# Optimization experiments

Measured on AMD Instinct MI355X. Metric: run time of the kernel, lower is better.

Reference implementation:

```python
import jax, jax.numpy as jnp
import numpy as np

B, C, H, W = 2, 64, 256, 256
G = 4  # groups in ResB convs


def _bn(x, g, b, m, v, eps=1e-5):
    inv = g / jnp.sqrt(v + eps)
    return x * inv[None, :, None, None] + (b - m * inv)[None, :, None, None]


def _gconv(x, w, b):
    y = jax.lax.conv_general_dilated(x, w, (1, 1), ((1, 1), (1, 1)),
                                     feature_group_count=G,
                                     dimension_numbers=('NCHW', 'OIHW', 'NCHW'))
    return y + b[None, :, None, None]


def _resb(x, w1, b1, w2, b2):
    h = jax.nn.leaky_relu(_gconv(x, w1, b1), 0.1)
    return _gconv(h, w2, b2) + x


def _conv1x1(x, w, b):
    return jnp.einsum('bchw,oc->bohw', x, w[:, :, 0, 0]) + b[None, :, None, None]


def _m_relax(M, num_pixels=2):
    # sum of M shifted by +/-1..num_pixels along the row (query) axis, zero padded
    out = M
    for i in range(1, num_pixels + 1):
        out = out + jnp.pad(M[:, :-i, :], ((0, 0), (i, 0), (0, 0)))
        out = out + jnp.pad(M[:, i:, :], ((0, 0), (0, i), (0, 0)))
    return out


def setup_inputs() -> dict:
    key = jax.random.key(0)
    ks = jax.random.split(key, 8)
    f = lambda k, shape, s=1.0: jax.random.normal(k, shape, dtype=jnp.float32) * s
    return {
        'x_left': f(ks[0], (B, C, H, W)),
        'x_right': f(ks[1], (B, C, H, W)),
        'catfea_left': f(ks[2], (B, C, H, W)),
        'catfea_right': f(ks[3], (B, C, H, W)),
        'bn_gamma': jnp.ones((C,), jnp.float32),
        'bn_beta': jnp.zeros((C,), jnp.float32),
        'bn_mean': jnp.zeros((C,), jnp.float32),
        'bn_var': jnp.ones((C,), jnp.float32),
        'rb_w1': f(ks[4], (C, C // G, 3, 3), 0.05),
        'rb_b1': jnp.zeros((C,), jnp.float32),
        'rb_w2': f(ks[5], (C, C // G, 3, 3), 0.05),
        'rb_b2': jnp.zeros((C,), jnp.float32),
        'bq_w': f(ks[6], (C, C, 1, 1), 0.05),
        'bq_b': jnp.zeros((C,), jnp.float32),
        'bs_w': f(ks[7], (C, C, 1, 1), 0.05),
        'bs_b': jnp.zeros((C,), jnp.float32),
    }


def reference(x_left, x_right, catfea_left, catfea_right,
              bn_gamma, bn_beta, bn_mean, bn_var,
              rb_w1, rb_b1, rb_w2, rb_b2,
              bq_w, bq_b, bs_w, bs_b):
    b, c0, h, w = x_left.shape

    Q = _conv1x1(_resb(_bn(x_left, bn_gamma, bn_beta, bn_mean, bn_var),
                       rb_w1, rb_b1, rb_w2, rb_b2), bq_w, bq_b)
    Q = Q - jnp.mean(Q, axis=3, keepdims=True)
    K = _conv1x1(_resb(_bn(x_right, bn_gamma, bn_beta, bn_mean, bn_var),
                       rb_w1, rb_b1, rb_w2, rb_b2), bs_w, bs_b)
    K = K - jnp.mean(K, axis=3, keepdims=True)

    c = Q.shape[1]
    # [b*h, w, c] and [b*h, c, w]  (w == w_size)
    Qr = Q.transpose(0, 2, 3, 1).reshape(-1, w, c)
    Kr = K.transpose(0, 2, 1, 3).reshape(-1, c, w)
    score = jnp.einsum('nic,ncj->nij', Qr, Kr)

    M_r2l = jax.nn.softmax(score, axis=-1)
    M_l2r = jax.nn.softmax(score.transpose(0, 2, 1), axis=-1)

    M_r2l_relaxed = _m_relax(M_r2l, 2)
    V_left = jax.lax.stop_gradient(
        jnp.einsum('nij,nji->ni', M_r2l_relaxed, M_l2r)).reshape(b, 1, h, w)
    M_l2r_relaxed = _m_relax(M_l2r, 2)
    V_right = jax.lax.stop_gradient(
        jnp.einsum('nij,nji->ni', M_l2r_relaxed, M_r2l)).reshape(b, 1, h, w)

    V_left_t = jnp.tanh(5.0 * V_left)
    V_right_t = jnp.tanh(5.0 * V_right)

    xr = x_right.transpose(0, 2, 3, 1).reshape(-1, w, c0)
    xl = x_left.transpose(0, 2, 3, 1).reshape(-1, w, c0)
    x_leftT = jnp.einsum('nij,njc->nic', M_r2l, xr).reshape(b, h, w, c0).transpose(0, 3, 1, 2)
    x_rightT = jnp.einsum('nij,njc->nic', M_l2r, xl).reshape(b, h, w, c0).transpose(0, 3, 1, 2)

    out_left = x_left * (1.0 - V_left_t) + x_leftT * V_left_t
    out_right = x_right * (1.0 - V_right_t) + x_rightT * V_right_t
    return out_left, out_right
```

## Files before the change

kernel.cpp:

```cpp
#include <hip/hip_runtime.h>
#include <math.h>

#define CC 64
#define HH 256
#define WW 256
#define GC 16
#define HWp (HH*WW)
#define LOG2E 1.44269504088896340736f

typedef __attribute__((ext_vector_type(8))) short short8;
typedef __attribute__((ext_vector_type(4))) float f32x4;
typedef __attribute__((ext_vector_type(2))) unsigned long u64x2;

static constexpr size_t OFS_BNSS = 0;
static constexpr size_t OFS_W1H  = 512;
static constexpr size_t OFS_W1L  = 20992;
static constexpr size_t OFS_W2H  = 41472;
static constexpr size_t OFS_W2L  = 61952;
static constexpr size_t OFS_WQH  = 82432;
static constexpr size_t OFS_WQL  = 98816;
static constexpr size_t OFS_WSH  = 115200;
static constexpr size_t OFS_WSL  = 131584;
static constexpr size_t OFS_RMAX = 147968;
static constexpr size_t OFS_RINV = OFS_RMAX + 524288;
static constexpr size_t OFS_CMAX = OFS_RINV + 524288;
static constexpr size_t OFS_CINV = OFS_CMAX + 524288;
static constexpr size_t OFS_XBNH = OFS_CINV + 524288;
static constexpr size_t HALO_BYTES = (size_t)2*258*258*64*2;
static constexpr size_t OFS_XBNL = OFS_XBNH + HALO_BYTES;
static constexpr size_t OFS_HH   = OFS_XBNL + HALO_BYTES;
static constexpr size_t OFS_HL   = OFS_HH   + HALO_BYTES;
static constexpr size_t OFS_QH   = OFS_HL   + HALO_BYTES;
static constexpr size_t QK_BYTES = (size_t)512*256*64*2;
static constexpr size_t OFS_QL   = OFS_QH + QK_BYTES;
static constexpr size_t OFS_KH   = OFS_QL + QK_BYTES;
static constexpr size_t OFS_KL   = OFS_KH + QK_BYTES;

__device__ __forceinline__ unsigned short f2bf(float v) {
    unsigned int u = __float_as_uint(v);
    return (unsigned short)((u + 0x7fffu + ((u >> 16) & 1u)) >> 16);
}
__device__ __forceinline__ float bf2f(unsigned short h) {
    return __uint_as_float(((unsigned int)h) << 16);
}

__global__ __launch_bounds__(256) void wprep(const float* __restrict__ g, const float* __restrict__ be,
        const float* __restrict__ mn, const float* __restrict__ va,
        const float* __restrict__ w1, const float* __restrict__ w2,
        const float* __restrict__ wq, const float* __restrict__ wsW,
        float* __restrict__ bnss,
        unsigned short* __restrict__ w1h, unsigned short* __restrict__ w1l,
// ... 16 lines not shown
        }
        unsigned short h1 = f2bf(v1), h2 = f2bf(v2);
        w1h[idx] = h1; w1l[idx] = f2bf(v1 - bf2f(h1));
        w2h[idx] = h2; w2l[idx] = f2bf(v2 - bf2f(h2));
    }
    for (int idx = t; idx < 64*128; idx += 256) {
        int oc = idx >> 7, k = idx & 127;
        float vq = wq[oc*64 + (k & 63)];
        float vs = wsW[oc*64 + (k & 63)];
        unsigned short hq = f2bf(vq), hs = f2bf(vs);
        wqh[idx] = hq; wql[idx] = f2bf(vq - bf2f(hq));
        wsh[idx] = hs; wsl[idx] = f2bf(vs - bf2f(hs));
    }
}

__global__ void zero_k(u64x2* __restrict__ p, size_t n) {
    size_t i = (size_t)blockIdx.x*blockDim.x + threadIdx.x;
    size_t st = (size_t)gridDim.x*blockDim.x;
    for (; i < n; i += st) p[i] = (u64x2){0ul, 0ul};
}

__global__ __launch_bounds__(256) void prep_k(const float* __restrict__ x,
        const float* __restrict__ bnss,
        unsigned short* __restrict__ xh, unsigned short* __restrict__ xl) {
    __shared__ float ld[64*256];
    __shared__ float sc[64], sh[64];
    int blk = blockIdx.x;
    int y = blk & 255, b = blk >> 8;
    int t = threadIdx.x;
    if (t < 64) { sc[t] = bnss[t]; sh[t] = bnss[64+t]; }
    for (int idx = t; idx < 16384; idx += 256) {
        int c = idx >> 8, xx = idx & 255;
        ld[c*256 + xx] = x[((size_t)(b*64 + c)*256 + y)*256 + xx];
    }
    __syncthreads();
    int px = t;
    size_t base = ((size_t)(b*258 + y+1)*258 + px+1)*64;
    #pragma unroll
    for (int ch = 0; ch < 4; ++ch) {
        short8 h0, h1, l0, l1;
        #pragma unroll
        for (int j = 0; j < 8; ++j) {
            int c = ch*16 + j;
            float f = ld[c*256 + px]*sc[c] + sh[c];
            unsigned short hh = f2bf(f);
            h0[j] = (short)hh; l0[j] = (short)f2bf(f - bf2f(hh));
        }
        #pragma unroll
        for (int j = 0; j < 8; ++j) {
            int c = ch*16 + 8 + j;
            float f = ld[c*256 + px]*sc[c] + sh[c];
            unsigned short hh = f2bf(f);
            h1[j] = (short)hh; l1[j] = (short)f2bf(f - bf2f(hh));
        }
        *(short8*)(xh + base + ch*16)     = h0;
        *(short8*)(xh + base + ch*16 + 8) = h1;
        *(short8*)(xl + base + ch*16)     = l0;
        *(short8*)(xl + base + ch*16 + 8) = l1;
    }
}

__global__ __launch_bounds__(256) void conv1_m(
        const unsigned short* __restrict__ inh, const unsigned short* __restrict__ inl,
        const unsigned short* __restrict__ wth, const unsigned short* __restrict__ wtl,
        const float* __restrict__ bias,
        unsigned short* __restrict__ oh, unsigned short* __restrict__ ol) {
    __shared__ unsigned short lh[256*72];
    __shared__ unsigned short ll[256*72];
    int blk = blockIdx.x;
    int y = blk & 255, b = blk >> 8;
    int t = threadIdx.x;
    int w = t >> 6, l = t & 63;
    int lr = l & 15, lg = l >> 4;

    f32x4 acc[4][4];
    #pragma unroll
    for (int g = 0; g < 4; ++g) {
        float bb = bias[g*16 + lr];
        #pragma unroll
        for (int mt = 0; mt < 4; ++mt) acc[mt][g] = (f32x4){bb,bb,bb,bb};
    }
    size_t lanebase = ((size_t)(b*258 + y)*258 + 64*w + lr)*64 + (lg & 1)*8;
    int koff[5];
    #pragma unroll
    for (int ks = 0; ks < 5; ++ks) {
        int tap = 2*ks + (lg >> 1);
        if (tap > 8) tap = 8;
        koff[ks] = ((tap/3)*258 + (tap%3))*64;
    }
    #pragma unroll
    for (int ks = 0; ks < 5; ++ks) {
        #pragma unroll
        for (int g = 0; g < 4; ++g) {
            short8 bh = *(const short8*)(wth + (g*16+lr)*160 + ks*32 + lg*8);
            short8 bl = *(const short8*)(wtl + (g*16+lr)*160 + ks*32 + lg*8);
            #pragma unroll
            for (int mt = 0; mt < 4; ++mt) {
                size_t off = lanebase + koff[ks] + mt*1024 + g*16;
                short8 ah = *(const short8*)(inh + off);
                short8 al = *(const short8*)(inl + off);
                acc[mt][g] = __builtin_amdgcn_mfma_f32_16x16x32_bf16(ah, bh, acc[mt][g], 0,0,0);
                acc[mt][g] = __builtin_amdgcn_mfma_f32_16x16x32_bf16(ah, bl, acc[mt][g], 0,0,0);
                acc[mt][g] = __builtin_amdgcn_mfma_f32_16x16x32_bf16(al, bh, acc[mt][g], 0,0,0);
            }
        }
    }
    #pragma unroll
    for (int mt = 0; mt < 4; ++mt)
        #pragma unroll
        for (int g = 0; g < 4; ++g)
            #pragma unroll
            for (int r = 0; r < 4; ++r) {
                float v = acc[mt][g][r];
                v = v > 0.f ? v : 0.1f*v;
                int px = 64*w + mt*16 + lg*4 + r;
                int oc = g*16 + lr;
                unsigned short hh = f2bf(v);
                lh[px*72 + oc] = hh;
                ll[px*72 + oc] = f2bf(v - bf2f(hh));
            }
    __syncthreads();
    size_t rowbase = ((size_t)(b*258 + y+1)*258 + 1)*64;
    #pragma unroll
    for (int i = 0; i < 8; ++i) {
        int cid = i*256 + t;
        int px = cid >> 3, part = cid & 7;
        *(short8*)(oh + rowbase + (size_t)px*64 + part*8) = *(short8*)&lh[px*72 + part*8];
        *(short8*)(ol + rowbase + (size_t)px*64 + part*8) = *(short8*)&ll[px*72 + part*8];
    }
}

__global__ __launch_bounds__(256) void conv2_m(
        const unsigned short* __restrict__ hh, const unsigned short* __restrict__ hl,
        const unsigned short* __restrict__ xbh, const unsigned short* __restrict__ xbl,
        const unsigned short* __restrict__ wth, const unsigned short* __restrict__ wtl,
        const float* __restrict__ bias2,
        const unsigned short* __restrict__ wph, const unsigned short* __restrict__ wpl,
        const float* __restrict__ biasq, float scaleOut,
        unsigned short* __restrict__ Qh, unsigned short* __restrict__ Ql) {
    __shared__ unsigned short rs[4*9216];
    __shared__ float red2[256];
    __shared__ float meanl[64];
    int blk = blockIdx.x;
    int y = blk & 255, b = blk >> 8;
    int t = threadIdx.x;
    int w = t >> 6, l = t & 63;
    int lr = l & 15, lg = l >> 4;

    f32x4 acc[4][4];
    #pragma unroll
    for (int g = 0; g < 4; ++g) {
        float bb = bias2[g*16 + lr];
        #pragma unroll
        for (int mt = 0; mt < 4; ++mt) acc[mt][g] = (f32x4){bb,bb,bb,bb};
    }
    size_t lanebase = ((size_t)(b*258 + y)*258 + 64*w + lr)*64 + (lg & 1)*8;
    int koff[5];
    #pragma unroll
    for (int ks = 0; ks < 5; ++ks) {
        int tap = 2*ks + (lg >> 1);
        if (tap > 8) tap = 8;
        koff[ks] = ((tap/3)*258 + (tap%3))*64;
    }
    #pragma unroll
    for (int ks = 0; ks < 5; ++ks) {
        #pragma unroll
        for (int g = 0; g < 4; ++g) {
            short8 bh = *(const short8*)(wth + (g*16+lr)*160 + ks*32 + lg*8);
            short8 bl = *(const short8*)(wtl + (g*16+lr)*160 + ks*32 + lg*8);
            #pragma unroll
            for (int mt = 0; mt < 4; ++mt) {
                size_t off = lanebase + koff[ks] + mt*1024 + g*16;
                short8 ah = *(const short8*)(hh + off);
                short8 al = *(const short8*)(hl + off);
                acc[mt][g] = __builtin_amdgcn_mfma_f32_16x16x32_bf16(ah, bh, acc[mt][g], 0,0,0);
                acc[mt][g] = __builtin_amdgcn_mfma_f32_16x16x32_bf16(ah, bl, acc[mt][g], 0,0,0);
                acc[mt][g] = __builtin_amdgcn_mfma_f32_16x16x32_bf16(al, bh, acc[mt][g], 0,0,0);
            }
        }
    }
    unsigned short* rsw = rs + w*9216;
    #pragma unroll
    for (int mt = 0; mt < 4; ++mt)
        #pragma unroll
        for (int g = 0; g < 4; ++g)
            #pragma unroll
            for (int r = 0; r < 4; ++r) {
                float v = acc[mt][g][r];
                int pxl = mt*16 + lg*4 + r;
                int oc = g*16 + lr;
                unsigned short hv = f2bf(v);
                rsw[pxl*72 + oc] = hv;
                rsw[4608 + pxl*72 + oc] = f2bf(v - bf2f(hv));
            }
    f32x4 acc2[4][4];
    #pragma unroll
    for (int nt = 0; nt < 4; ++nt) {
        float bb = biasq[nt*16 + lr];
        #pragma unroll
        for (int mt = 0; mt < 4; ++mt) acc2[mt][nt] = (f32x4){bb,bb,bb,bb};
    }
    size_t cbase = ((size_t)(b*258 + y+1)*258 + 64*w + lr + 1)*64 + lg*8;
    #pragma unroll
    for (int ks = 0; ks < 4; ++ks) {
        short8 Ah[4], Al[4];
        #pragma unroll
        for (int mt = 0; mt < 4; ++mt) {
            if (ks < 2) {
                Ah[mt] = *(short8*)&rsw[(mt*16+lr)*72 + ks*32 + lg*8];
                Al[mt] = *(short8*)&rsw[4608 + (mt*16+lr)*72 + ks*32 + lg*8];
            } else {
                size_t off = cbase + (size_t)mt*1024 + (ks-2)*32;
                Ah[mt] = *(const short8*)(xbh + off);
                Al[mt] = *(const short8*)(xbl + off);
            }
        }
        #pragma unroll
        for (int nt = 0; nt < 4; ++nt) {
            short8 Bh = *(const short8*)(wph + (nt*16+lr)*128 + ks*32 + lg*8);
            short8 Bl = *(const short8*)(wpl + (nt*16+lr)*128 + ks*32 + lg*8);
            #pragma unroll
            for (int mt = 0; mt < 4; ++mt) {
                acc2[mt][nt] = __builtin_amdgcn_mfma_f32_16x16x32_bf16(Ah[mt], Bh, acc2[mt][nt], 0,0,0);
                acc2[mt][nt] = __builtin_amdgcn_mfma_f32_16x16x32_bf16(Ah[mt], Bl, acc2[mt][nt], 0,0,0);
                acc2[mt][nt] = __builtin_amdgcn_mfma_f32_16x16x32_bf16(Al[mt], Bh, acc2[mt][nt], 0,0,0);
            }
        }
    }
    __syncthreads();
    float* qs = (float*)rs;
    #pragma unroll
    for (int mt = 0; mt < 4; ++mt)
        #pragma unroll
        for (int nt = 0; nt < 4; ++nt)
            #pragma unroll
            for (int r = 0; r < 4; ++r)
                qs[(64*w + mt*16 + lg*4 + r)*68 + nt*16 + lr] = acc2[mt][nt][r];
    __syncthreads();
    {
        int c = t & 63, seg = t >> 6;
        float s = 0.f;
        for (int i = 0; i < 64; ++i) s += qs[(seg*64 + i)*68 + c];
        red2[t] = s;
    }
    __syncthreads();
    if (t < 64) meanl[t] = (red2[t] + red2[64+t] + red2[128+t] + red2[192+t]) * (1.f/256.f);
    __syncthreads();
    int n = b*256 + y;
    size_t obase = ((size_t)n*256 + t)*64;
    #pragma unroll
    for (int ch = 0; ch < 4; ++ch) {
        short8 h0, h1, l0, l1;
        #pragma unroll
        for (int j = 0; j < 8; ++j) {
            int c = ch*16 + j;
            float f = (qs[t*68 + c] - meanl[c]) * scaleOut;
            unsigned short hv = f2bf(f);
            h0[j] = (short)hv; l0[j] = (short)f2bf(f - bf2f(hv));
        }
        #pragma unroll
        for (int j = 0; j < 8; ++j) {
            int c = ch*16 + 8 + j;
            float f = (qs[t*68 + c] - meanl[c]) * scaleOut;
            unsigned short hv = f2bf(f);
            h1[j] = (short)hv; l1[j] = (short)f2bf(f - bf2f(hv));
        }
        *(short8*)(Qh + obase + ch*16)     = h0;
        *(short8*)(Qh + obase + ch*16 + 8) = h1;
        *(short8*)(Ql + obase + ch*16)     = l0;
        *(short8*)(Ql + obase + ch*16 + 8) = l1;
    }
}

__global__ __launch_bounds__(256) void s1_stats(
        const unsigned short* __restrict__ Qhi, const unsigned short* __restrict__ Qlo,
        const unsigned short* __restrict__ Khi, const unsigned short* __restrict__ Klo,
        float* __restrict__ rmax, float* __restrict__ rinv,
        float* __restrict__ cmax, float* __restrict__ cinv) {
    __shared__ float colred[4][256][2];
    int n = blockIdx.x;
    int t = threadIdx.x;
    int w = t >> 6, l = t & 63;
    int lr = l & 15, lg = l >> 4;
    const size_t qb = (size_t)n * 16384;

    short8 qh[4][2], ql[4][2];
    #pragma unroll
    for (int rf = 0; rf < 4; ++rf)
        #pragma unroll
        for (int ks = 0; ks < 2; ++ks) {
            size_t a = qb + (size_t)(w*64 + rf*16 + lr)*64 + ks*32 + lg*8;
            qh[rf][ks] = *reinterpret_cast<const short8*>(Qhi + a);
            ql[rf][ks] = *reinterpret_cast<const short8*>(Qlo + a);
        }
    float mrow[4][4], srow[4][4];
    #pragma unroll
    for (int rf = 0; rf < 4; ++rf)
        #pragma unroll
        for (int r = 0; r < 4; ++r) { mrow[rf][r] = -3.0e38f; srow[rf][r] = 0.f; }

    for (int jt = 0; jt < 8; ++jt) {
        short8 kh[2][2], kl[2][2];
        #pragma unroll
        for (int cf = 0; cf < 2; ++cf)
            #pragma unroll
            for (int ks = 0; ks < 2; ++ks) {
                size_t a = qb + (size_t)(jt*32 + cf*16 + lr)*64 + ks*32 + lg*8;
                kh[cf][ks] = *reinterpret_cast<const short8*>(Khi + a);
                kl[cf][ks] = *reinterpret_cast<const short8*>(Klo + a);
            }
        f32x4 acc[4][2];
        #pragma unroll
        for (int rf = 0; rf < 4; ++rf)
            #pragma unroll
            for (int cf = 0; cf < 2; ++cf) acc[rf][cf] = (f32x4){0.f,0.f,0.f,0.f};
        #pragma unroll
        for (int ks = 0; ks < 2; ++ks)
            #pragma unroll
            for (int rf = 0; rf < 4; ++rf)
                #pragma unroll
                for (int cf = 0; cf < 2; ++cf) {
                    acc[rf][cf] = __builtin_amdgcn_mfma_f32_16x16x32_bf16(qh[rf][ks], kh[cf][ks], acc[rf][cf], 0,0,0);
                    acc[rf][cf] = __builtin_amdgcn_mfma_f32_16x16x32_bf16(qh[rf][ks], kl[cf][ks], acc[rf][cf], 0,0,0);
                    acc[rf][cf] = __builtin_amdgcn_mfma_f32_16x16x32_bf16(ql[rf][ks], kh[cf][ks], acc[rf][cf], 0,0,0);
                }
        #pragma unroll
        for (int rf = 0; rf < 4; ++rf)
            #pragma unroll
            for (int r = 0; r < 4; ++r) {
                float e0 = acc[rf][0][r], e1 = acc[rf][1][r];
                float m2 = fmaxf(mrow[rf][r], fmaxf(e0, e1));
                srow[rf][r] = srow[rf][r]*exp2f(mrow[rf][r]-m2) + exp2f(e0-m2) + exp2f(e1-m2);
                mrow[rf][r] = m2;
            }
        #pragma unroll
        for (int cf = 0; cf < 2; ++cf) {
            float m = acc[0][cf][0];
            #pragma unroll
            for (int rf = 0; rf < 4; ++rf)
                #pragma unroll
                for (int r = 0; r < 4; ++r) m = fmaxf(m, acc[rf][cf][r]);
            float s = 0.f;
            #pragma unroll
            for (int rf = 0; rf < 4; ++rf)
                #pragma unroll
                for (int r = 0; r < 4; ++r) s += exp2f(acc[rf][cf][r] - m);
            #pragma unroll
            for (int mask = 16; mask <= 32; mask <<= 1) {
                float om = __shfl_xor(m, mask);
                float os = __shfl_xor(s, mask);
                float m2 = fmaxf(m, om);
                s = s*exp2f(m-m2) + os*exp2f(om-m2);
                m = m2;
            }
            if (lg == 0) {
                int j = jt*32 + cf*16 + lr;
                colred[w][j][0] = m;
                colred[w][j][1] = s;
            }
        }
    }
    #pragma unroll
    for (int rf = 0; rf < 4; ++rf)
        #pragma unroll
        for (int r = 0; r < 4; ++r) {
            float m = mrow[rf][r], s = srow[rf][r];
            #pragma unroll
            for (int mask = 1; mask <= 8; mask <<= 1) {
                float om = __shfl_xor(m, mask);
                float os = __shfl_xor(s, mask);
                float m2 = fmaxf(m, om);
                s = s*exp2f(m-m2) + os*exp2f(om-m2);
                m = m2;
            }
            if (lr == 0) {
                int row = w*64 + rf*16 + lg*4 + r;
                rmax[n*256 + row] = m;
                rinv[n*256 + row] = 1.f / s;
            }
        }
    __syncthreads();
    {
        int j = t;
        float m = colred[0][j][0], s = colred[0][j][1];
        #pragma unroll
        for (int w2_ = 1; w2_ < 4; ++w2_) {
            float om = colred[w2_][j][0], os = colred[w2_][j][1];
            float m2 = fmaxf(m, om);
            s = s*exp2f(m-m2) + os*exp2f(om-m2);
            m = m2;
        }
        cmax[n*256 + j] = m;
        cinv[n*256 + j] = 1.f / s;
    }
}

__global__ __launch_bounds__(256) void s23_apply(
        const unsigned short* __restrict__ Ahi, const unsigned short* __restrict__ Alo,
        const unsigned short* __restrict__ Bhi, const unsigned short* __restrict__ Blo,
        const float* __restrict__ rowmax, const float* __restrict__ rowinv,
        const float* __restrict__ colmax, const float* __restrict__ colinv,
        const float* __restrict__ Xpv, const float* __restrict__ Xblend,
        float* __restrict__ outp) {
    __shared__ unsigned short pa[256][40];
    __shared__ unsigned short pb[256][40];
    __shared__ float vred[4][256];
    __shared__ float cmax_l[256], cinv_l[256];
    __shared__ float vfin[256];
    int n = blockIdx.x;
    int y = n & 255, b = n >> 8;
    int t = threadIdx.x;
    int w = t >> 6, l = t & 63;
    int lr = l & 15, lg = l >> 4;
    const size_t qb = (size_t)n * 16384;

    cmax_l[t] = colmax[n*256 + t];
    cinv_l[t] = colinv[n*256 + t];
    for (int q = t; q < 1024; q += 256) ((float*)vred)[q] = 0.f;

    float rmx[4][4], rin[4][4];
    #pragma unroll
    for (int rf = 0; rf < 4; ++rf)
        #pragma unroll
        for (int r = 0; r < 4; ++r) {
            int row = w*64 + rf*16 + lg*4 + r;
            rmx[rf][r] = rowmax[n*256 + row];
            rin[rf][r] = rowinv[n*256 + row];
        }
    short8 ah[4][2], al[4][2];
    #pragma unroll
    for (int rf = 0; rf < 4; ++rf)
        #pragma unroll
        for (int ks = 0; ks < 2; ++ks) {
            size_t a = qb + (size_t)(w*64 + rf*16 + lr)*64 + ks*32 + lg*8;
            ah[rf][ks] = *reinterpret_cast<const short8*>(Ahi + a);
            al[rf][ks] = *reinterpret_cast<const short8*>(Alo + a);
        }
    f32x4 pv[4][4];
    #pragma unroll
    for (int rf = 0; rf < 4; ++rf)
        #pragma unroll
        for (int cf = 0; cf < 4; ++cf) pv[rf][cf] = (f32x4){0.f,0.f,0.f,0.f};
    float vacc[6];
    #pragma unroll
    for (int s = 0; s < 6; ++s) vacc[s] = 0.f;

    const float* xpvb = Xpv + (size_t)b*CC*HWp + (size_t)y*WW;
    __syncthreads();

    for (int jt = 0; jt < 8; ++jt) {
        short8 bh[2][2], bl[2][2];
        #pragma unroll
        for (int cf = 0; cf < 2; ++cf)
            #pragma unroll
            for (int ks = 0; ks < 2; ++ks) {
                size_t a = qb + (size_t)(jt*32 + cf*16 + lr)*64 + ks*32 + lg*8;
                bh[cf][ks] = *reinterpret_cast<const short8*>(Bhi + a);
                bl[cf][ks] = *reinterpret_cast<const short8*>(Blo + a);
            }
        f32x4 acc[4][2];
        #pragma unroll
        for (int rf = 0; rf < 4; ++rf)
            #pragma unroll
            for (int cf = 0; cf < 2; ++cf) acc[rf][cf] = (f32x4){0.f,0.f,0.f,0.f};
        #pragma unroll
        for (int ks = 0; ks < 2; ++ks)
            #pragma unroll
            for (int rf = 0; rf < 4; ++rf)
                #pragma unroll
                for (int cf = 0; cf < 2; ++cf) {
                    acc[rf][cf] = __builtin_amdgcn_mfma_f32_16x16x32_bf16(ah[rf][ks], bh[cf][ks], acc[rf][cf], 0,0,0);
                    acc[rf][cf] = __builtin_amdgcn_mfma_f32_16x16x32_bf16(ah[rf][ks], bl[cf][ks], acc[rf][cf], 0,0,0);
                    acc[rf][cf] = __builtin_amdgcn_mfma_f32_16x16x32_bf16(al[rf][ks], bh[cf][ks], acc[rf][cf], 0,0,0);
                }
        #pragma unroll
        for (int rf = 0; rf < 4; ++rf)
            #pragma unroll
            for (int cf = 0; cf < 2; ++cf) {
                int col = cf*16 + lr;
                float cm = cmax_l[jt*32 + col];
                float ci = cinv_l[jt*32 + col];
                #pragma unroll
                for (int r = 0; r < 4; ++r) {
                    float e = acc[rf][cf][r];
                    int row = w*64 + rf*16 + lg*4 + r;
                    pa[row][col] = f2bf(exp2f(e - rmx[rf][r]) * rin[rf][r]);
                    pb[row][col] = f2bf(exp2f(e - cm) * ci);
                }
            }
        __syncthreads();
        #pragma unroll
        for (int Tl = 0; Tl < 4; ++Tl) {
            int T = w*4 + Tl;
            short8 afr = *reinterpret_cast<short8*>(&pa[T*16 + lr][lg*8]);
            #pragma unroll
            for (int dT = -1; dT <= 1; ++dT) {
                int Tp = T + dT;
                if (Tp < 0 || Tp > 15) continue;
                short8 bfr = *reinterpret_cast<short8*>(&pb[Tp*16 + lr][lg*8]);
                f32x4 wacc = (f32x4){0.f,0.f,0.f,0.f};
                wacc = __builtin_amdgcn_mfma_f32_16x16x32_bf16(afr, bfr, wacc, 0,0,0);
                #pragma unroll
                for (int r = 0; r < 4; ++r) {
                    int diff = lg*4 + r - lr - 16*dT;
                    if (diff >= -2 && diff <= 2) vacc[Tl + dT + 1] += wacc[r];
                }
            }
        }
        #pragma unroll
        for (int cf4 = 0; cf4 < 4; ++cf4) {
            const float* xp = xpvb + (size_t)(cf4*16 + lr)*HWp + jt*32 + lg*8;
            float4 xv0 = *(const float4*)(xp);
            float4 xv1 = *(const float4*)(xp + 4);
            short8 xf;
            xf[0] = (short)f2bf(xv0.x); xf[1] = (short)f2bf(xv0.y);
            xf[2] = (short)f2bf(xv0.z); xf[3] = (short)f2bf(xv0.w);
            xf[4] = (short)f2bf(xv1.x); xf[5] = (short)f2bf(xv1.y);
            xf[6] = (short)f2bf(xv1.z); xf[7] = (short)f2bf(xv1.w);
            #pragma unroll
            for (int rf = 0; rf < 4; ++rf) {
                short8 paf = *reinterpret_cast<short8*>(&pa[w*64 + rf*16 + lr][lg*8]);
                pv[rf][cf4] = __builtin_amdgcn_mfma_f32_16x16x32_bf16(paf, xf, pv[rf][cf4], 0,0,0);
            }
        }
        __syncthreads();
    }
    #pragma unroll
    for (int s = 0; s < 6; ++s) {
        float v = vacc[s];
        v += __shfl_xor(v, 16);
        v += __shfl_xor(v, 32);
        if (lg == 0) {
            int i = (w*4 - 1 + s)*16 + lr;
            if (i >= 0 && i < 256) vred[w][i] = v;
        }
    }
    __syncthreads();
    vfin[t] = tanhf(5.f * (vred[0][t] + vred[1][t] + vred[2][t] + vred[3][t]));
    __syncthreads();
    const float* xbb = Xblend + (size_t)b*CC*HWp + (size_t)y*WW;
    float* ob = outp + (size_t)b*CC*HWp + (size_t)y*WW;
    #pragma unroll
    for (int rf = 0; rf < 4; ++rf)
        #pragma unroll
        for (int r = 0; r < 4; ++r) {
            int row = w*64 + rf*16 + lg*4 + r;
            float vt = vfin[row];
            #pragma unroll
            for (int cf4 = 0; cf4 < 4; ++cf4) {
                int c = cf4*16 + lr;
                size_t ga = (size_t)c*HWp + row;
                float xv = xbb[ga];
                ob[ga] = xv + vt * (pv[rf][cf4][r] - xv);
            }
        }
}

extern "C" void kernel_launch(void* const* d_in, const int* in_sizes, int n_in,
                              void* d_out, int out_size, void* d_ws, size_t ws_size,
                              hipStream_t stream) {
    const float* x_left  = (const float*)d_in[0];
    const float* x_right = (const float*)d_in[1];
    const float* bn_g = (const float*)d_in[4];
    const float* bn_b = (const float*)d_in[5];
    const float* bn_m = (const float*)d_in[6];
    const float* bn_v = (const float*)d_in[7];
    const float* w1  = (const float*)d_in[8];
    const float* b1  = (const float*)d_in[9];
// ... 14 lines not shown
    unsigned short* wql = (unsigned short*)(base + OFS_WQL);
    unsigned short* wsh = (unsigned short*)(base + OFS_WSH);
    unsigned short* wsl = (unsigned short*)(base + OFS_WSL);
    float* rmaxp = (float*)(base + OFS_RMAX);
    float* rinvp = (float*)(base + OFS_RINV);
    float* cmaxp = (float*)(base + OFS_CMAX);
    float* cinvp = (float*)(base + OFS_CINV);
    unsigned short* xbh = (unsigned short*)(base + OFS_XBNH);
    unsigned short* xbl = (unsigned short*)(base + OFS_XBNL);
    unsigned short* hh  = (unsigned short*)(base + OFS_HH);
    unsigned short* hl  = (unsigned short*)(base + OFS_HL);
    unsigned short* Qh  = (unsigned short*)(base + OFS_QH);
    unsigned short* Ql  = (unsigned short*)(base + OFS_QL);
    unsigned short* Kh  = (unsigned short*)(base + OFS_KH);
    unsigned short* Kl  = (unsigned short*)(base + OFS_KL);

    float* outl = (float*)d_out;
    float* outr = outl + (size_t)2*CC*HWp;

    hipLaunchKernelGGL(wprep, dim3(1), dim3(256), 0, stream,
                       bn_g, bn_b, bn_m, bn_v, w1, w2, bqw, bsw,
                       bnss, w1h, w1l, w2h, w2l, wqh, wql, wsh, wsl);
    hipLaunchKernelGGL(zero_k, dim3(2048), dim3(256), 0, stream,
                       (u64x2*)(base + OFS_XBNH), (size_t)(4*HALO_BYTES/16));
    hipLaunchKernelGGL(prep_k,  dim3(512), dim3(256), 0, stream, x_left, bnss, xbh, xbl);
    hipLaunchKernelGGL(conv1_m, dim3(512), dim3(256), 0, stream, xbh, xbl, w1h, w1l, b1, hh, hl);
    hipLaunchKernelGGL(conv2_m, dim3(512), dim3(256), 0, stream, hh, hl, xbh, xbl,
                       w2h, w2l, b2, wqh, wql, bqb, LOG2E, Qh, Ql);
    hipLaunchKernelGGL(prep_k,  dim3(512), dim3(256), 0, stream, x_right, bnss, xbh, xbl);
    hipLaunchKernelGGL(conv1_m, dim3(512), dim3(256), 0, stream, xbh, xbl, w1h, w1l, b1, hh, hl);
    hipLaunchKernelGGL(conv2_m, dim3(512), dim3(256), 0, stream, hh, hl, xbh, xbl,
                       w2h, w2l, b2, wsh, wsl, bsb, 1.0f, Kh, Kl);
    hipLaunchKernelGGL(s1_stats, dim3(512), dim3(256), 0, stream, Qh, Ql, Kh, Kl, rmaxp, rinvp, cmaxp, cinvp);
    hipLaunchKernelGGL(s23_apply, dim3(512), dim3(256), 0, stream,
                       Qh, Ql, Kh, Kl, rmaxp, rinvp, cmaxp, cinvp, x_right, x_left, outl);
    hipLaunchKernelGGL(s23_apply, dim3(512), dim3(256), 0, stream,
                       Kh, Kl, Qh, Ql, cmaxp, cinvp, rmaxp, rinvp, x_left, x_right, outr);
}
```

Before: 703.6 us.

## Use 512-thread blocks, zero only halo borders, precompute bf16 inputs for PV

```diff
diff --git a/kernel.cpp b/kernel.cpp
--- a/kernel.cpp
+++ b/kernel.cpp
@@ -10,7 +10,6 @@
 
 typedef __attribute__((ext_vector_type(8))) short short8;
 typedef __attribute__((ext_vector_type(4))) float f32x4;
-typedef __attribute__((ext_vector_type(2))) unsigned long u64x2;
 
 static constexpr size_t OFS_BNSS = 0;
 static constexpr size_t OFS_W1H  = 512;
@@ -27,6 +26,7 @@
 static constexpr size_t OFS_CINV = OFS_CMAX + 524288;
 static constexpr size_t OFS_XBNH = OFS_CINV + 524288;
 static constexpr size_t HALO_BYTES = (size_t)2*258*258*64*2;
+static constexpr size_t HALO_U16  = HALO_BYTES/2;
 static constexpr size_t OFS_XBNL = OFS_XBNH + HALO_BYTES;
 static constexpr size_t OFS_HH   = OFS_XBNL + HALO_BYTES;
 static constexpr size_t OFS_HL   = OFS_HH   + HALO_BYTES;
@@ -35,6 +35,9 @@
 static constexpr size_t OFS_QL   = OFS_QH + QK_BYTES;
 static constexpr size_t OFS_KH   = OFS_QL + QK_BYTES;
 static constexpr size_t OFS_KL   = OFS_KH + QK_BYTES;
+static constexpr size_t XB_BYTES = (size_t)2*64*256*256*2;
+static constexpr size_t OFS_XLB  = OFS_KL + QK_BYTES;
+static constexpr size_t OFS_XRB  = OFS_XLB + XB_BYTES;
 
 __device__ __forceinline__ unsigned short f2bf(float v) {
     unsigned int u = __float_as_uint(v);
@@ -81,53 +84,68 @@
     }
 }
 
-__global__ void zero_k(u64x2* __restrict__ p, size_t n) {
-    size_t i = (size_t)blockIdx.x*blockDim.x + threadIdx.x;
-    size_t st = (size_t)gridDim.x*blockDim.x;
-    for (; i < n; i += st) p[i] = (u64x2){0ul, 0ul};
-}
-
-__global__ __launch_bounds__(256) void prep_k(const float* __restrict__ x,
+__global__ __launch_bounds__(256) void zhalo(unsigned short* __restrict__ p) {
+    int idx = blockIdx.x*256 + threadIdx.x;
+    if (idx >= 65792) return;
+    int ch8 = idx & 7;
+    int rest = idx >> 3;
+    int slab = rest / 1028;
+    int pos  = rest % 1028;
+    size_t slabbase = (size_t)slab * 4260096;
+    int y, x;
+    if (pos < 258)      { y = 0;   x = pos; }
+    else if (pos < 516) { y = 257; x = pos - 258; }
+    else if (pos < 772) { y = pos - 516 + 1; x = 0; }
+    else                { y = pos - 772 + 1; x = 257; }
+    size_t off = slabbase + ((size_t)y*258 + x)*64 + ch8*8;
+    *(short8*)(p + off) = (short8){0,0,0,0,0,0,0,0};
+}
+
+__global__ __launch_bounds__(512) void prep_k(const float* __restrict__ x,
         const float* __restrict__ bnss,
-        unsigned short* __restrict__ xh, unsigned short* __restrict__ xl) {
+        unsigned short* __restrict__ xh, unsigned short* __restrict__ xl,
+        unsigned short* __restrict__ xb16) {
     __shared__ float ld[64*256];
     __shared__ float sc[64], sh[64];
     int blk = blockIdx.x;
     int y = blk & 255, b = blk >> 8;
     int t = threadIdx.x;
     if (t < 64) { sc[t] = bnss[t]; sh[t] = bnss[64+t]; }
-    for (int idx = t; idx < 16384; idx += 256) {
+    for (int idx = t; idx < 16384; idx += 512) {
         int c = idx >> 8, xx = idx & 255;
-        ld[c*256 + xx] = x[((size_t)(b*64 + c)*256 + y)*256 + xx];
-    }
-    __syncthreads();
-    int px = t;
+        float v = x[((size_t)(b*64 + c)*256 + y)*256 + xx];
+        ld[c*256 + xx] = v;
+        xb16[((size_t)(b*64 + c)*256 + y)*256 + xx] = f2bf(v);
+    }
+    __syncthreads();
+    int px = t >> 1, half = (t & 1) * 32;
     size_t base = ((size_t)(b*258 + y+1)*258 + px+1)*64;
     #pragma unroll
-    for (int ch = 0; ch < 4; ++ch) {
+    for (int cc = 0; cc < 2; ++cc) {
+        int cb = half + cc*16;
         short8 h0, h1, l0, l1;
         #pragma unroll
         for (int j = 0; j < 8; ++j) {
-            int c = ch*16 + j;
+            int c = cb + j;
             float f = ld[c*256 + px]*sc[c] + sh[c];
             unsigned short hh = f2bf(f);
             h0[j] = (short)hh; l0[j] = (short)f2bf(f - bf2f(hh));
         }
         #pragma unroll
         for (int j = 0; j < 8; ++j) {
-            int c = ch*16 + 8 + j;
+            int c = cb + 8 + j;
             float f = ld[c*256 + px]*sc[c] + sh[c];
             unsigned short hh = f2bf(f);
             h1[j] = (short)hh; l1[j] = (short)f2bf(f - bf2f(hh));
         }
-        *(short8*)(xh + base + ch*16)     = h0;
-        *(short8*)(xh + base + ch*16 + 8) = h1;
-        *(short8*)(xl + base + ch*16)     = l0;
-        *(short8*)(xl + base + ch*16 + 8) = l1;
-    }
-}
-
-__global__ __launch_bounds__(256) void conv1_m(
+        *(short8*)(xh + base + cb)     = h0;
+        *(short8*)(xh + base + cb + 8) = h1;
+        *(short8*)(xl + base + cb)     = l0;
+        *(short8*)(xl + base + cb + 8) = l1;
+    }
+}
+
+__global__ __launch_bounds__(512) void conv1_m(
         const unsigned short* __restrict__ inh, const unsigned short* __restrict__ inl,
         const unsigned short* __restrict__ wth, const unsigned short* __restrict__ wtl,
         const float* __restrict__ bias,
@@ -140,14 +158,14 @@
     int w = t >> 6, l = t & 63;
     int lr = l & 15, lg = l >> 4;
 
-    f32x4 acc[4][4];
+    f32x4 acc[2][4];
     #pragma unroll
     for (int g = 0; g < 4; ++g) {
         float bb = bias[g*16 + lr];
         #pragma unroll
-        for (int mt = 0; mt < 4; ++mt) acc[mt][g] = (f32x4){bb,bb,bb,bb};
-    }
-    size_t lanebase = ((size_t)(b*258 + y)*258 + 64*w + lr)*64 + (lg & 1)*8;
+        for (int mt = 0; mt < 2; ++mt) acc[mt][g] = (f32x4){bb,bb,bb,bb};
+    }
+    size_t lanebase = ((size_t)(b*258 + y)*258 + 32*w + lr)*64 + (lg & 1)*8;
     int koff[5];
     #pragma unroll
     for (int ks = 0; ks < 5; ++ks) {
@@ -162,7 +180,7 @@
             short8 bh = *(const short8*)(wth + (g*16+lr)*160 + ks*32 + lg*8);
             short8 bl = *(const short8*)(wtl + (g*16+lr)*160 + ks*32 + lg*8);
             #pragma unroll
-            for (int mt = 0; mt < 4; ++mt) {
+            for (int mt = 0; mt < 2; ++mt) {
                 size_t off = lanebase + koff[ks] + mt*1024 + g*16;
                 short8 ah = *(const short8*)(inh + off);
                 short8 al = *(const short8*)(inl + off);
@@ -173,14 +191,14 @@
         }
     }
     #pragma unroll
-    for (int mt = 0; mt < 4; ++mt)
+    for (int mt = 0; mt < 2; ++mt)
         #pragma unroll
         for (int g = 0; g < 4; ++g)
             #pragma unroll
             for (int r = 0; r < 4; ++r) {
                 float v = acc[mt][g][r];
                 v = v > 0.f ? v : 0.1f*v;
-                int px = 64*w + mt*16 + lg*4 + r;
+                int px = 32*w + mt*16 + lg*4 + r;
                 int oc = g*16 + lr;
                 unsigned short hh = f2bf(v);
                 lh[px*72 + oc] = hh;
@@ -189,15 +207,15 @@
     __syncthreads();
     size_t rowbase = ((size_t)(b*258 + y+1)*258 + 1)*64;
     #pragma unroll
-    for (int i = 0; i < 8; ++i) {
-        int cid = i*256 + t;
+    for (int i = 0; i < 4; ++i) {
+        int cid = i*512 + t;
         int px = cid >> 3, part = cid & 7;
         *(short8*)(oh + rowbase + (size_t)px*64 + part*8) = *(short8*)&lh[px*72 + part*8];
         *(short8*)(ol + rowbase + (size_t)px*64 + part*8) = *(short8*)&ll[px*72 + part*8];
     }
 }
 
-__global__ __launch_bounds__(256) void conv2_m(
+__global__ __launch_bounds__(512) void conv2_m(
         const unsigned short* __restrict__ hh, const unsigned short* __restrict__ hl,
         const unsigned short* __restrict__ xbh, const unsigned short* __restrict__ xbl,
         const unsigned short* __restrict__ wth, const unsigned short* __restrict__ wtl,
@@ -205,8 +223,8 @@
         const unsigned short* __restrict__ wph, const unsigned short* __restrict__ wpl,
         const float* __restrict__ biasq, float scaleOut,
         unsigned short* __restrict__ Qh, unsigned short* __restrict__ Ql) {
-    __shared__ unsigned short rs[4*9216];
-    __shared__ float red2[256];
+    __shared__ unsigned short rs[8*4608];
+    __shared__ float red2[512];
     __shared__ float meanl[64];
     int blk = blockIdx.x;
     int y = blk & 255, b = blk >> 8;
@@ -214,14 +232,14 @@
     int w = t >> 6, l = t & 63;
     int lr = l & 15, lg = l >> 4;
 
-    f32x4 acc[4][4];
+    f32x4 acc[2][4];
     #pragma unroll
     for (int g = 0; g < 4; ++g) {
         float bb = bias2[g*16 + lr];
         #pragma unroll
-        for (int mt = 0; mt < 4; ++mt) acc[mt][g] = (f32x4){bb,bb,bb,bb};
-    }
-    size_t lanebase = ((size_t)(b*258 + y)*258 + 64*w + lr)*64 + (lg & 1)*8;
+        for (int mt = 0; mt < 2; ++mt) acc[mt][g] = (f32x4){bb,bb,bb,bb};
+    }
+    size_t lanebase = ((size_t)(b*258 + y)*258 + 32*w + lr)*64 + (lg & 1)*8;
     int koff[5];
     #pragma unroll
     for (int ks = 0; ks < 5; ++ks) {
@@ -236,7 +254,7 @@
             short8 bh = *(const short8*)(wth + (g*16+lr)*160 + ks*32 + lg*8);
             short8 bl = *(const short8*)(wtl + (g*16+lr)*160 + ks*32 + lg*8);
             #pragma unroll
-            for (int mt = 0; mt < 4; ++mt) {
+            for (int mt = 0; mt < 2; ++mt) {
                 size_t off = lanebase + koff[ks] + mt*1024 + g*16;
                 short8 ah = *(const short8*)(hh + off);
                 short8 al = *(const short8*)(hl + off);
@@ -246,9 +264,9 @@
             }
         }
     }
-    unsigned short* rsw = rs + w*9216;
-    #pragma unroll
-    for (int mt = 0; mt < 4; ++mt)
+    unsigned short* rsw = rs + w*4608;
+    #pragma unroll
+    for (int mt = 0; mt < 2; ++mt)
         #pragma unroll
         for (int g = 0; g < 4; ++g)
             #pragma unroll
@@ -258,24 +276,24 @@
                 int oc = g*16 + lr;
                 unsigned short hv = f2bf(v);
                 rsw[pxl*72 + oc] = hv;
-                rsw[4608 + pxl*72 + oc] = f2bf(v - bf2f(hv));
-            }
-    f32x4 acc2[4][4];
+                rsw[2304 + pxl*72 + oc] = f2bf(v - bf2f(hv));
+            }
+    f32x4 acc2[2][4];
     #pragma unroll
     for (int nt = 0; nt < 4; ++nt) {
         float bb = biasq[nt*16 + lr];
         #pragma unroll
-        for (int mt = 0; mt < 4; ++mt) acc2[mt][nt] = (f32x4){bb,bb,bb,bb};
-    }
-    size_t cbase = ((size_t)(b*258 + y+1)*258 + 64*w + lr + 1)*64 + lg*8;
+        for (int mt = 0; mt < 2; ++mt) acc2[mt][nt] = (f32x4){bb,bb,bb,bb};
+    }
+    size_t cbase = ((size_t)(b*258 + y+1)*258 + 32*w + lr + 1)*64 + lg*8;
     #pragma unroll
     for (int ks = 0; ks < 4; ++ks) {
-        short8 Ah[4], Al[4];
-        #pragma unroll
-        for (int mt = 0; mt < 4; ++mt) {
+        short8 Ah[2], Al[2];
+        #pragma unroll
+        for (int mt = 0; mt < 2; ++mt) {
             if (ks < 2) {
                 Ah[mt] = *(short8*)&rsw[(mt*16+lr)*72 + ks*32 + lg*8];
-                Al[mt] = *(short8*)&rsw[4608 + (mt*16+lr)*72 + ks*32 + lg*8];
+                Al[mt] = *(short8*)&rsw[2304 + (mt*16+lr)*72 + ks*32 + lg*8];
             } else {
                 size_t off = cbase + (size_t)mt*1024 + (ks-2)*32;
                 Ah[mt] = *(const short8*)(xbh + off);
@@ -287,7 +305,7 @@
             short8 Bh = *(const short8*)(wph + (nt*16+lr)*128 + ks*32 + lg*8);
             short8 Bl = *(const short8*)(wpl + (nt*16+lr)*128 + ks*32 + lg*8);
             #pragma unroll
-            for (int mt = 0; mt < 4; ++mt) {
+            for (int mt = 0; mt < 2; ++mt) {
                 acc2[mt][nt] = __builtin_amdgcn_mfma_f32_16x16x32_bf16(Ah[mt], Bh, acc2[mt][nt], 0,0,0);
                 acc2[mt][nt] = __builtin_amdgcn_mfma_f32_16x16x32_bf16(Ah[mt], Bl, acc2[mt][nt], 0,0,0);
                 acc2[mt][nt] = __builtin_amdgcn_mfma_f32_16x16x32_bf16(Al[mt], Bh, acc2[mt][nt], 0,0,0);
@@ -297,72 +315,79 @@
     __syncthreads();
     float* qs = (float*)rs;
     #pragma unroll
-    for (int mt = 0; mt < 4; ++mt)
+    for (int mt = 0; mt < 2; ++mt)
         #pragma unroll
         for (int nt = 0; nt < 4; ++nt)
             #pragma unroll
             for (int r = 0; r < 4; ++r)
-                qs[(64*w + mt*16 + lg*4 + r)*68 + nt*16 + lr] = acc2[mt][nt][r];
+                qs[(32*w + mt*16 + lg*4 + r)*68 + nt*16 + lr] = acc2[mt][nt][r];
     __syncthreads();
     {
         int c = t & 63, seg = t >> 6;
         float s = 0.f;
-        for (int i = 0; i < 64; ++i) s += qs[(seg*64 + i)*68 + c];
+        for (int i = 0; i < 32; ++i) s += qs[(seg*32 + i)*68 + c];
         red2[t] = s;
     }
     __syncthreads();
-    if (t < 64) meanl[t] = (red2[t] + red2[64+t] + red2[128+t] + red2[192+t]) * (1.f/256.f);
+    if (t < 64) {
+        float s = 0.f;
+        #pragma unroll
+        for (int seg = 0; seg < 8; ++seg) s += red2[seg*64 + t];
+        meanl[t] = s * (1.f/256.f);
+    }
     __syncthreads();
     int n = b*256 + y;
-    size_t obase = ((size_t)n*256 + t)*64;
-    #pragma unroll
-    for (int ch = 0; ch < 4; ++ch) {
+    int px = t >> 1, half = (t & 1) * 32;
+    size_t obase = ((size_t)n*256 + px)*64;
+    #pragma unroll
+    for (int cc = 0; cc < 2; ++cc) {
+        int cb = half + cc*16;
         short8 h0, h1, l0, l1;
         #pragma unroll
         for (int j = 0; j < 8; ++j) {
-            int c = ch*16 + j;
-            float f = (qs[t*68 + c] - meanl[c]) * scaleOut;
+            int c = cb + j;
+            float f = (qs[px*68 + c] - meanl[c]) * scaleOut;
             unsigned short hv = f2bf(f);
             h0[j] = (short)hv; l0[j] = (short)f2bf(f - bf2f(hv));
         }
         #pragma unroll
         for (int j = 0; j < 8; ++j) {
-            int c = ch*16 + 8 + j;
-            float f = (qs[t*68 + c] - meanl[c]) * scaleOut;
+            int c = cb + 8 + j;
+            float f = (qs[px*68 + c] - meanl[c]) * scaleOut;
             unsigned short hv = f2bf(f);
             h1[j] = (short)hv; l1[j] = (short)f2bf(f - bf2f(hv));
         }
-        *(short8*)(Qh + obase + ch*16)     = h0;
-        *(short8*)(Qh + obase + ch*16 + 8) = h1;
-        *(short8*)(Ql + obase + ch*16)     = l0;
-        *(short8*)(Ql + obase + ch*16 + 8) = l1;
-    }
-}
-
-__global__ __launch_bounds__(256) void s1_stats(
+        *(short8*)(Qh + obase + cb)     = h0;
+        *(short8*)(Qh + obase + cb + 8) = h1;
+        *(short8*)(Ql + obase + cb)     = l0;
+        *(short8*)(Ql + obase + cb + 8) = l1;
+    }
+}
+
+__global__ __launch_bounds__(512) void s1_stats(
         const unsigned short* __restrict__ Qhi, const unsigned short* __restrict__ Qlo,
         const unsigned short* __restrict__ Khi, const unsigned short* __restrict__ Klo,
         float* __restrict__ rmax, float* __restrict__ rinv,
         float* __restrict__ cmax, float* __restrict__ cinv) {
-    __shared__ float colred[4][256][2];
+    __shared__ float colred[8][256][2];
     int n = blockIdx.x;
     int t = threadIdx.x;
     int w = t >> 6, l = t & 63;
     int lr = l & 15, lg = l >> 4;
     const size_t qb = (size_t)n * 16384;
 
-    short8 qh[4][2], ql[4][2];
-    #pragma unroll
-    for (int rf = 0; rf < 4; ++rf)
+    short8 qh[2][2], ql[2][2];
+    #pragma unroll
+    for (int rf = 0; rf < 2; ++rf)
         #pragma unroll
         for (int ks = 0; ks < 2; ++ks) {
-            size_t a = qb + (size_t)(w*64 + rf*16 + lr)*64 + ks*32 + lg*8;
+            size_t a = qb + (size_t)(w*32 + rf*16 + lr)*64 + ks*32 + lg*8;
             qh[rf][ks] = *reinterpret_cast<const short8*>(Qhi + a);
             ql[rf][ks] = *reinterpret_cast<const short8*>(Qlo + a);
         }
-    float mrow[4][4], srow[4][4];
-    #pragma unroll
-    for (int rf = 0; rf < 4; ++rf)
+    float mrow[2][4], srow[2][4];
+    #pragma unroll
+    for (int rf = 0; rf < 2; ++rf)
         #pragma unroll
         for (int r = 0; r < 4; ++r) { mrow[rf][r] = -3.0e38f; srow[rf][r] = 0.f; }
 
@@ -376,15 +401,15 @@
                 kh[cf][ks] = *reinterpret_cast<const short8*>(Khi + a);
                 kl[cf][ks] = *reinterpret_cast<const short8*>(Klo + a);
             }
-        f32x4 acc[4][2];
-        #pragma unroll
-        for (int rf = 0; rf < 4; ++rf)
+        f32x4 acc[2][2];
+        #pragma unroll
+        for (int rf = 0; rf < 2; ++rf)
             #pragma unroll
             for (int cf = 0; cf < 2; ++cf) acc[rf][cf] = (f32x4){0.f,0.f,0.f,0.f};
         #pragma unroll
         for (int ks = 0; ks < 2; ++ks)
             #pragma unroll
-            for (int rf = 0; rf < 4; ++rf)
+            for (int rf = 0; rf < 2; ++rf)
                 #pragma unroll
                 for (int cf = 0; cf < 2; ++cf) {
                     acc[rf][cf] = __builtin_amdgcn_mfma_f32_16x16x32_bf16(qh[rf][ks], kh[cf][ks], acc[rf][cf], 0,0,0);
@@ -392,7 +417,7 @@
                     acc[rf][cf] = __builtin_amdgcn_mfma_f32_16x16x32_bf16(ql[rf][ks], kh[cf][ks], acc[rf][cf], 0,0,0);
                 }
         #pragma unroll
-        for (int rf = 0; rf < 4; ++rf)
+        for (int rf = 0; rf < 2; ++rf)
             #pragma unroll
             for (int r = 0; r < 4; ++r) {
                 float e0 = acc[rf][0][r], e1 = acc[rf][1][r];
@@ -404,12 +429,12 @@
         for (int cf = 0; cf < 2; ++cf) {
             float m = acc[0][cf][0];
             #pragma unroll
-            for (int rf = 0; rf < 4; ++rf)
+            for (int rf = 0; rf < 2; ++rf)
                 #pragma unroll
                 for (int r = 0; r < 4; ++r) m = fmaxf(m, acc[rf][cf][r]);
             float s = 0.f;
             #pragma unroll
-            for (int rf = 0; rf < 4; ++rf)
+            for (int rf = 0; rf < 2; ++rf)
                 #pragma unroll
                 for (int r = 0; r < 4; ++r) s += exp2f(acc[rf][cf][r] - m);
             #pragma unroll
@@ -428,7 +453,7 @@
         }
     }
     #pragma unroll
-    for (int rf = 0; rf < 4; ++rf)
+    for (int rf = 0; rf < 2; ++rf)
         #pragma unroll
         for (int r = 0; r < 4; ++r) {
             float m = mrow[rf][r], s = srow[rf][r];
@@ -441,17 +466,17 @@
                 m = m2;
             }
             if (lr == 0) {
-                int row = w*64 + rf*16 + lg*4 + r;
+                int row = w*32 + rf*16 + lg*4 + r;
                 rmax[n*256 + row] = m;
                 rinv[n*256 + row] = 1.f / s;
             }
         }
     __syncthreads();
-    {
+    if (t < 256) {
         int j = t;
         float m = colred[0][j][0], s = colred[0][j][1];
         #pragma unroll
-        for (int w2_ = 1; w2_ < 4; ++w2_) {
+        for (int w2_ = 1; w2_ < 8; ++w2_) {
             float om = colred[w2_][j][0], os = colred[w2_][j][1];
             float m2 = fmaxf(m, om);
             s = s*exp2f(m-m2) + os*exp2f(om-m2);
@@ -462,16 +487,16 @@
     }
 }
 
-__global__ __launch_bounds__(256) void s23_apply(
+__global__ __launch_bounds__(512) void s23_apply(
         const unsigned short* __restrict__ Ahi, const unsigned short* __restrict__ Alo,
         const unsigned short* __restrict__ Bhi, const unsigned short* __restrict__ Blo,
         const float* __restrict__ rowmax, const float* __restrict__ rowinv,
         const float* __restrict__ colmax, const float* __restrict__ colinv,
-        const float* __restrict__ Xpv, const float* __restrict__ Xblend,
+        const unsigned short* __restrict__ Xpv16, const float* __restrict__ Xblend,
         float* __restrict__ outp) {
     __shared__ unsigned short pa[256][40];
     __shared__ unsigned short pb[256][40];
-    __shared__ float vred[4][256];
+    __shared__ float vred[8][256];
     __shared__ float cmax_l[256], cinv_l[256];
     __shared__ float vfin[256];
     int n = blockIdx.x;
@@ -481,38 +506,39 @@
     int lr = l & 15, lg = l >> 4;
     const size_t qb = (size_t)n * 16384;
 
-    cmax_l[t] = colmax[n*256 + t];
-    cinv_l[t] = colinv[n*256 + t];
-    for (int q = t; q < 1024; q += 256) ((float*)vred)[q] = 0.f;
-
-    float rmx[4][4], rin[4][4];
-    #pragma unroll
-    for (int rf = 0; rf < 4; ++rf)
+    if (t < 256) {
+        cmax_l[t] = colmax[n*256 + t];
+        cinv_l[t] = colinv[n*256 + t];
+    }
+    for (int q = t; q < 2048; q += 512) ((float*)vred)[q] = 0.f;
+
+    float rmx[2][4], rin[2][4];
+    #pragma unroll
+    for (int rf = 0; rf < 2; ++rf)
         #pragma unroll
         for (int r = 0; r < 4; ++r) {
-            int row = w*64 + rf*16 + lg*4 + r;
+            int row = w*32 + rf*16 + lg*4 + r;
             rmx[rf][r] = rowmax[n*256 + row];
             rin[rf][r] = rowinv[n*256 + row];
         }
-    short8 ah[4][2], al[4][2];
-    #pragma unroll
-    for (int rf = 0; rf < 4; ++rf)
+    short8 ah[2][2], al[2][2];
+    #pragma unroll
+    for (int rf = 0; rf < 2; ++rf)
         #pragma unroll
         for (int ks = 0; ks < 2; ++ks) {
-            size_t a = qb + (size_t)(w*64 + rf*16 + lr)*64 + ks*32 + lg*8;
+            size_t a = qb + (size_t)(w*32 + rf*16 + lr)*64 + ks*32 + lg*8;
             ah[rf][ks] = *reinterpret_cast<const short8*>(Ahi + a);
             al[rf][ks] = *reinterpret_cast<const short8*>(Alo + a);
         }
-    f32x4 pv[4][4];
-    #pragma unroll
-    for (int rf = 0; rf < 4; ++rf)
+    f32x4 pv[2][4];
+    #pragma unroll
+    for (int rf = 0; rf < 2; ++rf)
         #pragma unroll
         for (int cf = 0; cf < 4; ++cf) pv[rf][cf] = (f32x4){0.f,0.f,0.f,0.f};
-    float vacc[6];
-    #pragma unroll
-    for (int s = 0; s < 6; ++s) vacc[s] = 0.f;
-
-    const float* xpvb = Xpv + (size_t)b*CC*HWp + (size_t)y*WW;
+    float vacc[4];
+    #pragma unroll
+    for (int s = 0; s < 4; ++s) vacc[s] = 0.f;
+
     __syncthreads();
 
     for (int jt = 0; jt < 8; ++jt) {
@@ -525,15 +551,15 @@
                 bh[cf][ks] = *reinterpret_cast<const short8*>(Bhi + a);
                 bl[cf][ks] = *reinterpret_cast<const short8*>(Blo + a);
             }
-        f32x4 acc[4][2];
-        #pragma unroll
-        for (int rf = 0; rf < 4; ++rf)
+        f32x4 acc[2][2];
+        #pragma unroll
+        for (int rf = 0; rf < 2; ++rf)
             #pragma unroll
             for (int cf = 0; cf < 2; ++cf) acc[rf][cf] = (f32x4){0.f,0.f,0.f,0.f};
         #pragma unroll
         for (int ks = 0; ks < 2; ++ks)
             #pragma unroll
-            for (int rf = 0; rf < 4; ++rf)
+            for (int rf = 0; rf < 2; ++rf)
                 #pragma unroll
                 for (int cf = 0; cf < 2; ++cf) {
                     acc[rf][cf] = __builtin_amdgcn_mfma_f32_16x16x32_bf16(ah[rf][ks], bh[cf][ks], acc[rf][cf], 0,0,0);
@@ -541,7 +567,7 @@
                     acc[rf][cf] = __builtin_amdgcn_mfma_f32_16x16x32_bf16(al[rf][ks], bh[cf][ks], acc[rf][cf], 0,0,0);
                 }
         #pragma unroll
-        for (int rf = 0; rf < 4; ++rf)
+        for (int rf = 0; rf < 2; ++rf)
             #pragma unroll
             for (int cf = 0; cf < 2; ++cf) {
                 int col = cf*16 + lr;
@@ -550,15 +576,15 @@
                 #pragma unroll
                 for (int r = 0; r < 4; ++r) {
                     float e = acc[rf][cf][r];
-                    int row = w*64 + rf*16 + lg*4 + r;
-                    pa[row][col] = f2bf(exp2f(e - rmx[rf][r]) * rin[rf][r]);
+                    int row = w*32 + rf*16 + lg*4 + r;
+                    pa[row][col] = f2bf(exp2f(e - rmx[rf][r]));
                     pb[row][col] = f2bf(exp2f(e - cm) * ci);
                 }
             }
         __syncthreads();
         #pragma unroll
-        for (int Tl = 0; Tl < 4; ++Tl) {
-            int T = w*4 + Tl;
+        for (int Tl = 0; Tl < 2; ++Tl) {
+            int T = w*2 + Tl;
             short8 afr = *reinterpret_cast<short8*>(&pa[T*16 + lr][lg*8]);
             #pragma unroll
             for (int dT = -1; dT <= 1; ++dT) {
@@ -570,55 +596,54 @@
                 #pragma unroll
                 for (int r = 0; r < 4; ++r) {
                     int diff = lg*4 + r - lr - 16*dT;
-                    if (diff >= -2 && diff <= 2) vacc[Tl + dT + 1] += wacc[r];
+                    if (diff >= -2 && diff <= 2) vacc[Tl + dT + 1] += wacc[r] * rin[Tl][r];
                 }
             }
         }
         #pragma unroll
         for (int cf4 = 0; cf4 < 4; ++cf4) {
-            const float* xp = xpvb + (size_t)(cf4*16 + lr)*HWp + jt*32 + lg*8;
-            float4 xv0 = *(const float4*)(xp);
-            float4 xv1 = *(const float4*)(xp + 4);
-            short8 xf;
-            xf[0] = (short)f2bf(xv0.x); xf[1] = (short)f2bf(xv0.y);
-            xf[2] = (short)f2bf(xv0.z); xf[3] = (short)f2bf(xv0.w);
-            xf[4] = (short)f2bf(xv1.x); xf[5] = (short)f2bf(xv1.y);
-            xf[6] = (short)f2bf(xv1.z); xf[7] = (short)f2bf(xv1.w);
-            #pragma unroll
-            for (int rf = 0; rf < 4; ++rf) {
-                short8 paf = *reinterpret_cast<short8*>(&pa[w*64 + rf*16 + lr][lg*8]);
+            short8 xf = *(const short8*)(Xpv16 + (((size_t)(b*64 + cf4*16 + lr))*256 + y)*256 + jt*32 + lg*8);
+            #pragma unroll
+            for (int rf = 0; rf < 2; ++rf) {
+                short8 paf = *reinterpret_cast<short8*>(&pa[w*32 + rf*16 + lr][lg*8]);
                 pv[rf][cf4] = __builtin_amdgcn_mfma_f32_16x16x32_bf16(paf, xf, pv[rf][cf4], 0,0,0);
             }
         }
         __syncthreads();
     }
     #pragma unroll
-    for (int s = 0; s < 6; ++s) {
+    for (int s = 0; s < 4; ++s) {
         float v = vacc[s];
         v += __shfl_xor(v, 16);
         v += __shfl_xor(v, 32);
         if (lg == 0) {
-            int i = (w*4 - 1 + s)*16 + lr;
+            int i = (w*2 - 1 + s)*16 + lr;
             if (i >= 0 && i < 256) vred[w][i] = v;
         }
     }
     __syncthreads();
-    vfin[t] = tanhf(5.f * (vred[0][t] + vred[1][t] + vred[2][t] + vred[3][t]));
+    if (t < 256) {
+        float s = 0.f;
+        #pragma unroll
+        for (int ww = 0; ww < 8; ++ww) s += vred[ww][t];
+        vfin[t] = tanhf(5.f * s);
+    }
     __syncthreads();
     const float* xbb = Xblend + (size_t)b*CC*HWp + (size_t)y*WW;
     float* ob = outp + (size_t)b*CC*HWp + (size_t)y*WW;
     #pragma unroll
-    for (int rf = 0; rf < 4; ++rf)
+    for (int rf = 0; rf < 2; ++rf)
         #pragma unroll
         for (int r = 0; r < 4; ++r) {
-            int row = w*64 + rf*16 + lg*4 + r;
+            int row = w*32 + rf*16 + lg*4 + r;
             float vt = vfin[row];
+            float ri = rin[rf][r];
             #pragma unroll
             for (int cf4 = 0; cf4 < 4; ++cf4) {
                 int c = cf4*16 + lr;
                 size_t ga = (size_t)c*HWp + row;
                 float xv = xbb[ga];
-                ob[ga] = xv + vt * (pv[rf][cf4][r] - xv);
+                ob[ga] = xv + vt * (pv[rf][cf4][r]*ri - xv);
             }
         }
 }
@@ -663,6 +688,8 @@
     unsigned short* Ql  = (unsigned short*)(base + OFS_QL);
     unsigned short* Kh  = (unsigned short*)(base + OFS_KH);
     unsigned short* Kl  = (unsigned short*)(base + OFS_KL);
+    unsigned short* xlb = (unsigned short*)(base + OFS_XLB);
+    unsigned short* xrb = (unsigned short*)(base + OFS_XRB);
 
     float* outl = (float*)d_out;
     float* outr = outl + (size_t)2*CC*HWp;
@@ -670,19 +697,18 @@
     hipLaunchKernelGGL(wprep, dim3(1), dim3(256), 0, stream,
                        bn_g, bn_b, bn_m, bn_v, w1, w2, bqw, bsw,
                        bnss, w1h, w1l, w2h, w2l, wqh, wql, wsh, wsl);
-    hipLaunchKernelGGL(zero_k, dim3(2048), dim3(256), 0, stream,
-                       (u64x2*)(base + OFS_XBNH), (size_t)(4*HALO_BYTES/16));
-    hipLaunchKernelGGL(prep_k,  dim3(512), dim3(256), 0, stream, x_left, bnss, xbh, xbl);
-    hipLaunchKernelGGL(conv1_m, dim3(512), dim3(256), 0, stream, xbh, xbl, w1h, w1l, b1, hh, hl);
-    hipLaunchKernelGGL(conv2_m, dim3(512), dim3(256), 0, stream, hh, hl, xbh, xbl,
+    hipLaunchKernelGGL(zhalo, dim3(257), dim3(256), 0, stream, (unsigned short*)(base + OFS_XBNH));
+    hipLaunchKernelGGL(prep_k,  dim3(512), dim3(512), 0, stream, x_left, bnss, xbh, xbl, xlb);
+    hipLaunchKernelGGL(conv1_m, dim3(512), dim3(512), 0, stream, xbh, xbl, w1h, w1l, b1, hh, hl);
+    hipLaunchKernelGGL(conv2_m, dim3(512), dim3(512), 0, stream, hh, hl, xbh, xbl,
                        w2h, w2l, b2, wqh, wql, bqb, LOG2E, Qh, Ql);
-    hipLaunchKernelGGL(prep_k,  dim3(512), dim3(256), 0, stream, x_right, bnss, xbh, xbl);
-    hipLaunchKernelGGL(conv1_m, dim3(512), dim3(256), 0, stream, xbh, xbl, w1h, w1l, b1, hh, hl);
-    hipLaunchKernelGGL(conv2_m, dim3(512), dim3(256), 0, stream, hh, hl, xbh, xbl,
+    hipLaunchKernelGGL(prep_k,  dim3(512), dim3(512), 0, stream, x_right, bnss, xbh, xbl, xrb);
+    hipLaunchKernelGGL(conv1_m, dim3(512), dim3(512), 0, stream, xbh, xbl, w1h, w1l, b1, hh, hl);
+    hipLaunchKernelGGL(conv2_m, dim3(512), dim3(512), 0, stream, hh, hl, xbh, xbl,
                        w2h, w2l, b2, wsh, wsl, bsb, 1.0f, Kh, Kl);
-    hipLaunchKernelGGL(s1_stats, dim3(512), dim3(256), 0, stream, Qh, Ql, Kh, Kl, rmaxp, rinvp, cmaxp, cinvp);
-    hipLaunchKernelGGL(s23_apply, dim3(512), dim3(256), 0, stream,
-                       Qh, Ql, Kh, Kl, rmaxp, rinvp, cmaxp, cinvp, x_right, x_left, outl);
-    hipLaunchKernelGGL(s23_apply, dim3(512), dim3(256), 0, stream,
-                       Kh, Kl, Qh, Ql, cmaxp, cinvp, rmaxp, rinvp, x_left, x_right, outr);
-}
+    hipLaunchKernelGGL(s1_stats, dim3(512), dim3(512), 0, stream, Qh, Ql, Kh, Kl, rmaxp, rinvp, cmaxp, cinvp);
+    hipLaunchKernelGGL(s23_apply, dim3(512), dim3(512), 0, stream,
+                       Qh, Ql, Kh, Kl, rmaxp, rinvp, cmaxp, cinvp, xrb, x_left, outl);
+    hipLaunchKernelGGL(s23_apply, dim3(512), dim3(512), 0, stream,
+                       Kh, Kl, Qh, Ql, cmaxp, cinvp, rmaxp, rinvp, xlb, x_right, outr);
+}
```

Result: faster. 580.6 us (-17.5%).
